# Kernel optimization log

Hardware: AMD Instinct MI355X
Metric: run time of the kernel (lower is better)

## Reference

```python
import jax, jax.numpy as jnp
import numpy as np

B, N, D, H, F = 16, 512, 768, 8, 96  # D == H*F, dims preserved across layers
NEG_INF = -1e20


def setup_inputs() -> dict:
    key = jax.random.key(0)
    ks = jax.random.split(key, 16)
    embeddings = jax.random.normal(ks[0], (B, N, D), dtype=jnp.float32)
    # 0/1 float adjacency with self-loops so no row is fully masked
    adj = (jax.random.uniform(ks[1], (B, N, N)) < 0.3).astype(jnp.float32)
    adj = jnp.maximum(adj, jnp.eye(N, dtype=jnp.float32)[None])
    convo_len = jnp.full((B,), N, dtype=jnp.int32)

    def layer_params(k0, k1, k2, k3, k4, in_dim, out_dim):
        sW = (2.0 / (in_dim + out_dim)) ** 0.5  # ~xavier
        sa = (2.0 / (out_dim + 1)) ** 0.5
        sH = (2.0 / (in_dim + in_dim)) ** 0.5
        return dict(
            W=jax.random.normal(k0, (H, in_dim, out_dim)) * sW,
            b=jnp.zeros((out_dim,), jnp.float32),
            a_src=jax.random.normal(k1, (H, out_dim, 1)) * sa,
            a_dst=jax.random.normal(k2, (H, out_dim, 1)) * sa,
            Hw=jax.random.normal(k3, (in_dim, in_dim)) * sH,
            Hb=jnp.zeros((in_dim,), jnp.float32),
        )

    p0 = layer_params(ks[2], ks[3], ks[4], ks[5], ks[6], D, F)
    p1 = layer_params(ks[7], ks[8], ks[9], ks[10], ks[11], D, F)
    return {
        "embeddings": embeddings, "adj": adj, "convo_len": convo_len,
        "W0": p0["W"], "b0": p0["b"], "a_src0": p0["a_src"], "a_dst0": p0["a_dst"], "Hw0": p0["Hw"], "Hb0": p0["Hb"],
        "W1": p1["W"], "b1": p1["b"], "a_src1": p1["a_src"], "a_dst1": p1["a_dst"], "Hw1": p1["Hw"], "Hb1": p1["Hb"],
    }


def gat_layer(x, adj, W, b, a_src, a_dst, Hw, Hb):
    b_, n_, _ = x.shape
    h_, _, f_ = W.shape
    h = jnp.einsum('bni,hio->bhno', x, W)            # [B,H,N,F]
    t = jnp.tanh(h)
    s = jnp.einsum('bhno,ho->bhn', t, a_src[..., 0])  # attn_src
    d = jnp.einsum('bhno,ho->bhn', t, a_dst[..., 0])  # attn_dst
    attn = jax.nn.leaky_relu(s[:, :, :, None] + d[:, :, None, :], 0.2)  # [B,H,N,N]
    attn = jnp.where(adj[:, None, :, :] > 0, attn, NEG_INF)
    attn = jax.nn.softmax(attn, axis=-1)
    out = jnp.einsum('bhij,bhjo->bhio', attn, h) + b  # [B,H,N,F]
    # faithful to torch: transpose(0,1).contiguous().view(batch, N, -1)
    out = jnp.transpose(out, (1, 0, 2, 3)).reshape(b_, n_, h_ * f_)
    out = jax.nn.elu(out)
    gate = jax.nn.sigmoid(x @ Hw.T + Hb)
    return gate * out + (1.0 - gate) * x


def reference(embeddings, adj, convo_len,
              W0, b0, a_src0, a_dst0, Hw0, Hb0,
              W1, b1, a_src1, a_dst1, Hw1, Hb1):
    x = gat_layer(embeddings, adj, W0, b0, a_src0, a_dst0, Hw0, Hb0)
    x = gat_layer(x, adj, W1, b1, a_src1, a_dst1, Hw1, Hb1)
    return x
```

## Files before the change

### kernel.cpp

```cpp
#include <hip/hip_runtime.h>
#include <cstdint>
#include <cstddef>

typedef __attribute__((ext_vector_type(4))) float f32x4;
typedef __attribute__((ext_vector_type(8))) __bf16 bf16x8;
typedef __attribute__((ext_vector_type(8))) unsigned short u16x8;
typedef __attribute__((ext_vector_type(4))) unsigned short u16x4;

__device__ __forceinline__ unsigned short f2bf(float f){
  unsigned int u = __float_as_uint(f);
  u += 0x7fffu + ((u >> 16) & 1u);
  return (unsigned short)(u >> 16);
}
__device__ __forceinline__ float bf2f(unsigned short u){
  return __uint_as_float(((unsigned int)u) << 16);
}
__device__ __forceinline__ float fast_tanh(float x){
  const float e = __expf(2.f * x);
  return 1.f - 2.f / (e + 1.f);
}

__device__ __forceinline__ void gload_lds16(const void* g, void* l){
  __builtin_amdgcn_global_load_lds((const __attribute__((address_space(1))) void*)g,
                                   (__attribute__((address_space(3))) void*)l, 16, 0, 0);
}

__device__ __forceinline__ f32x4 mfma16(bf16x8 a, bf16x8 b, f32x4 c){
  return __builtin_amdgcn_mfma_f32_16x16x32_bf16(a, b, c, 0, 0, 0);
}

#define SBAR()  { __builtin_amdgcn_sched_barrier(0); __builtin_amdgcn_s_barrier(); __builtin_amdgcn_sched_barrier(0); }

__global__ __launch_bounds__(256) void prep_kernel(const float* __restrict__ in,
                                                   unsigned short* __restrict__ out,
                                                   const float* __restrict__ adj,
                                                   unsigned int* __restrict__ mask,
                                                   const float* __restrict__ W0,
                                                   const float* __restrict__ Hw0,
                                                   unsigned short* __restrict__ Bt0,
                                                   const float* __restrict__ W1,
                                                   const float* __restrict__ Hw1,
                                                   unsigned short* __restrict__ Bt1){
  const int bid = blockIdx.x;
  if (bid < 6144){
    int i = bid * 256 + threadIdx.x;
    f32x4 v = ((const f32x4*)in)[i];
    union { unsigned short u[4]; unsigned long long ll; } o;
    #pragma unroll
    for (int e = 0; e < 4; ++e) o.u[e] = f2bf(v[e]);
    ((unsigned long long*)out)[i] = o.ll;
  } else if (bid < 6656){
    int idx = (bid - 6144) * 256 + threadIdx.x;
    const float* a = adj + (size_t)idx * 32;
    unsigned int m = 0;
    #pragma unroll
    for (int e = 0; e < 8; ++e){
      f32x4 v = *(const f32x4*)(a + e * 4);
      m |= (v[0] > 0.f ? 1u : 0u) << (e * 4);
      m |= (v[1] > 0.f ? 1u : 0u) << (e * 4 + 1);
      m |= (v[2] > 0.f ? 1u : 0u) << (e * 4 + 2);
      m |= (v[3] > 0.f ? 1u : 0u) << (e * 4 + 3);
    }
    mask[idx] = m;
  } else {
    const int rel = bid - 6656;
    const int layer = rel >= 1536;
    const int n = layer ? rel - 1536 : rel;
    const float* W  = layer ? W1  : W0;
    const float* Hw = layer ? Hw1 : Hw0;
    unsigned short* Bt = layer ? Bt1 : Bt0;
    const int k4 = threadIdx.x;
    if (k4 < 192){
      float v[4];
      if (n < 768){
        int head = n / 96, f = n % 96;
        const float* base = W + (size_t)head * 768 * 96 + f;
        #pragma unroll
        for (int e = 0; e < 4; ++e) v[e] = base[(size_t)(k4 * 4 + e) * 96];
      } else {
        f32x4 t = *(const f32x4*)(Hw + (size_t)(n - 768) * 768 + k4 * 4);
        #pragma unroll
        for (int e = 0; e < 4; ++e) v[e] = t[e];
      }
      union { unsigned short u[4]; unsigned long long ll; } o;
      #pragma unroll
      for (int e = 0; e < 4; ++e) o.u[e] = f2bf(v[e]);
      ((unsigned long long*)(Bt + (size_t)n * 768))[k4] = o.ll;
    }
  }
}

__global__ __launch_bounds__(256, 3)
void gemm_kernel(const unsigned short* __restrict__ A,
                 const unsigned short* __restrict__ Bt,
                 const float* __restrict__ Hb,
                 unsigned short* __restrict__ hT,
                 unsigned short* __restrict__ glogit){
  __shared__ __align__(16) char lds[49152];
  const int tid  = threadIdx.x;
  const int wid  = tid >> 6;
  const int lane = tid & 63;
  const int orig = blockIdx.x;
  const int wgid = (orig & 7) * 192 + (orig >> 3);
  const int mtile = wgid / 24, ntile = wgid % 24;
  const int m0 = mtile * 128, n0 = ntile * 64;
  const int wm = (wid >> 1) * 64, wn = (wid & 1) * 32;
  const int g = lane >> 4, r16 = lane & 15;

  auto stage = [&](int kt, char* base){
    #pragma unroll
    for (int c = 0; c < 4; ++c){
      const int ch = c * 256 + tid;
      const int row = ch >> 3, sp = ch & 7;
      const int cj = sp ^ (row & 7);
      gload_lds16(A + (size_t)(m0 + row) * 768 + kt * 64 + cj * 8, base + ch * 16);
    }
    #pragma unroll
    for (int c = 0; c < 2; ++c){
      const int ch = c * 256 + tid;
      const int row = ch >> 3, sp = ch & 7;
      const int cj = sp ^ (row & 7);
      gload_lds16(Bt + (size_t)(n0 + row) * 768 + kt * 64 + cj * 8, base + 16384 + ch * 16);
    }
  };

  f32x4 acc[4][2];
  #pragma unroll
  for (int i = 0; i < 4; ++i)
    #pragma unroll
    for (int j = 0; j < 2; ++j) acc[i][j] = (f32x4){0.f, 0.f, 0.f, 0.f};

  stage(0, lds);
  stage(1, lds + 24576);

  for (int kt = 0; kt < 12; ++kt){
    if (kt < 11) { asm volatile("s_waitcnt vmcnt(6)" ::: "memory"); }
    else         { asm volatile("s_waitcnt vmcnt(0)" ::: "memory"); }
    SBAR();
    const char* base = lds + (kt & 1) * 24576;
    bf16x8 af[4][2], bfr[2][2];
    #pragma unroll
    for (int t = 0; t < 4; ++t){
      const int rowA = wm + t * 16 + r16;
      #pragma unroll
      for (int kk = 0; kk < 2; ++kk){
        const int ckk = (kk << 2) | g;
        af[t][kk] = *(const bf16x8*)(base + rowA * 128 + ((ckk ^ (rowA & 7)) << 4));
      }
    }
    #pragma unroll
    for (int nt = 0; nt < 2; ++nt){
      const int rowB = wn + nt * 16 + r16;
      #pragma unroll
      for (int kk = 0; kk < 2; ++kk){
        const int ckk = (kk << 2) | g;
        bfr[nt][kk] = *(const bf16x8*)(base + 16384 + rowB * 128 + ((ckk ^ (rowB & 7)) << 4));
      }
    }
    __builtin_amdgcn_s_setprio(1);
    #pragma unroll
    for (int mt = 0; mt < 4; ++mt)
      #pragma unroll
      for (int nt = 0; nt < 2; ++nt){
        acc[mt][nt] = mfma16(af[mt][0], bfr[nt][0], acc[mt][nt]);
        acc[mt][nt] = mfma16(af[mt][1], bfr[nt][1], acc[mt][nt]);
      }
    __builtin_amdgcn_s_setprio(0);
    SBAR();
    if (kt < 10) stage(kt + 2, lds + (kt & 1) * 24576);
  }

  if (n0 < 768){
    #pragma unroll
    for (int mt = 0; mt < 4; ++mt){
      #pragma unroll
      for (int nt = 0; nt < 2; ++nt){
        const int n_local = wn + nt * 16 + r16;
        const int m_base  = wm + mt * 16 + g * 4;
        union { unsigned short u[4]; unsigned long long ll; } pk;
        #pragma unroll
        for (int r = 0; r < 4; ++r) pk.u[r] = f2bf(acc[mt][nt][r]);
        const int byte = m_base * 2;
        const int chunk = byte >> 4, o = byte & 15;
        const int pbyte = n_local * 256 + ((chunk ^ (n_local & 15)) << 4) + o;
        *(unsigned long long*)(lds + pbyte) = pk.ll;
      }
    }
    __syncthreads();
    const int b_ = m0 >> 9, nodebase = m0 & 511;
    #pragma unroll
    for (int it = 0; it < 4; ++it){
      const int ci = it * 256 + tid;
      const int row = ci >> 4, l = ci & 15;
      const int pbyte = row * 256 + (((l ^ (row & 15))) << 4);
      f32x4 v = *(const f32x4*)(lds + pbyte);
      const int n = n0 + row, head = n / 96, f = n % 96;
      *(f32x4*)(hT + (((size_t)(b_ * 8 + head)) * 96 + f) * 512 + nodebase + l * 8) = v;
    }
  } else {
    #pragma unroll
    for (int mt = 0; mt < 4; ++mt){
      #pragma unroll
      for (int nt = 0; nt < 2; ++nt){
        const int n_local = wn + nt * 16 + r16;
        const float hbv = Hb[n0 - 768 + n_local];
        const int c = n_local >> 3;
        #pragma unroll
        for (int r = 0; r < 4; ++r){
          const int m_local = wm + mt * 16 + g * 4 + r;
          const int pbyte = m_local * 128 + ((c ^ (m_local & 7)) << 4) + (n_local & 7) * 2;
          *(unsigned short*)(lds + pbyte) = f2bf(acc[mt][nt][r] + hbv);
        }
      }
    }
    __syncthreads();
    const int colbase = n0 - 768;
    #pragma unroll
    for (int it = 0; it < 4; ++it){
      const int ci = it * 256 + tid;
      const int row = ci >> 3, l = ci & 7;
      const int pbyte = row * 128 + ((l ^ (row & 7)) << 4);
      f32x4 v = *(const f32x4*)(lds + pbyte);
      *(f32x4*)(glogit + (size_t)(m0 + row) * 768 + colbase + l * 8) = v;
    }
  }
}

__global__ __launch_bounds__(256)
void sd_kernel(const unsigned short* __restrict__ hT, const float* __restrict__ asrc,
               const float* __restrict__ adst, float* __restrict__ s, float* __restrict__ d){
  const int bh = blockIdx.x;
  const int tid = threadIdx.x;
  const int head = bh & 7;
  __shared__ float as_lds[96], ad_lds[96];
  if (tid < 96) as_lds[tid] = asrc[head * 96 + tid];
  else if (tid >= 128 && tid < 224) ad_lds[tid - 128] = adst[head * 96 + tid - 128];
  __syncthreads();

  const unsigned short* hTb = hT + (size_t)bh * 96 * 512 + tid * 2;
  float s0 = 0.f, s1 = 0.f, d0 = 0.f, d1 = 0.f;
  #pragma unroll 8
  for (int f = 0; f < 96; ++f){
    const unsigned int u = *(const unsigned int*)(hTb + (size_t)f * 512);
    const float t0 = fast_tanh(bf2f((unsigned short)(u & 0xffffu)));
    const float t1 = fast_tanh(bf2f((unsigned short)(u >> 16)));
    const float a = as_lds[f], dd = ad_lds[f];
    s0 += t0 * a;  s1 += t1 * a;
    d0 += t0 * dd; d1 += t1 * dd;
  }
  const int o = (bh << 9) + tid * 2;
  *(float2*)(s + o) = make_float2(s0, s1);
  *(float2*)(d + o) = make_float2(d0, d1);
}

__global__ __launch_bounds__(256)
void attn_kernel(const float* __restrict__ s, const float* __restrict__ d,
                 const unsigned int* __restrict__ mask,
                 const unsigned short* __restrict__ hT,
                 const float* __restrict__ bias,
                 const unsigned short* __restrict__ glogit,
                 const float* __restrict__ xin,
                 float* __restrict__ outf,
                 unsigned short* __restrict__ outb,
                 int write_b){
  const int idx = blockIdx.x;
  const int bh = idx & 127, ib = idx >> 7;
  const int b  = bh >> 3;
  const int tid = threadIdx.x, wid = tid >> 6, lane = tid & 63;
  const int g = lane >> 4, r16 = lane & 15;
  const int rowbase = ib * 64 + wid * 16;

  __shared__ float d_lds[512];
  __shared__ float bias_lds[96];
  __shared__ __align__(16) char vbuf[3][12288];
  float* att_s = (float*)vbuf;

  const float* dv = d + bh * 512;
  if (tid < 128) ((f32x4*)d_lds)[tid] = ((const f32x4*)dv)[tid];
  if (tid >= 128 && tid < 152) ((f32x4*)bias_lds)[tid - 128] = ((const f32x4*)bias)[tid - 128];

  const unsigned short* hTb = hT + (size_t)bh * 96 * 512;

  auto stage = [&](int p, int bufi){
    #pragma unroll
    for (int ss2 = 0; ss2 < 3; ++ss2){
      const int ch = ss2 * 256 + tid;
      const int row = ch >> 3, slotpos = ch & 7;
      const int cj = slotpos ^ (row & 7);
      gload_lds16(hTb + (size_t)row * 512 + p * 64 + cj * 8, vbuf[bufi] + ch * 16);
    }
  };

  const int i_mine = rowbase + r16;
  const float s_i = s[bh * 512 + i_mine];

  unsigned int mw[16];
  {
    const uint4* mrow = (const uint4*)(mask + ((size_t)b * 512 + i_mine) * 16);
    uint4 a0 = mrow[0], a1 = mrow[1], a2 = mrow[2], a3 = mrow[3];
    mw[0]=a0.x; mw[1]=a0.y; mw[2]=a0.z; mw[3]=a0.w;
    mw[4]=a1.x; mw[5]=a1.y; mw[6]=a1.z; mw[7]=a1.w;
    mw[8]=a2.x; mw[9]=a2.y; mw[10]=a2.z; mw[11]=a2.w;
    mw[12]=a3.x; mw[13]=a3.y; mw[14]=a3.z; mw[15]=a3.w;
  }

  stage(0, 0);
  stage(1, 1);
  asm volatile("s_waitcnt lgkmcnt(0)" ::: "memory");

  float m_i;
  f32x4 acc2[6];
  #pragma unroll
  for (int ft = 0; ft < 6; ++ft) acc2[ft] = (f32x4){0.f, 0.f, 0.f, 0.f};
  float L0 = 0.f, L1 = 0.f, L2 = 0.f, L3 = 0.f;

  #pragma unroll
  for (int p = 0; p < 8; ++p){
    if (p < 7) { asm volatile("s_waitcnt vmcnt(3)" ::: "memory"); }
    else       { asm volatile("s_waitcnt vmcnt(0)" ::: "memory"); }
    SBAR();
    if (p == 0){
      float Mx = d_lds[lane];
      #pragma unroll
      for (int t = 1; t < 8; ++t) Mx = fmaxf(Mx, d_lds[t * 64 + lane]);
      #pragma unroll
      for (int o = 32; o > 0; o >>= 1) Mx = fmaxf(Mx, __shfl_xor(Mx, o));
      const float scm = s_i + Mx;
      m_i = fmaxf(scm, 0.2f * scm);
    }
    if (p < 6) stage(p + 2, (p + 2) % 3);
    const char* vb = vbuf[p % 3];
    #pragma unroll
    for (int half = 0; half < 2; ++half){
      const int jt = p * 2 + half;
      const unsigned int w = mw[jt];
      const int j8 = jt * 32 + g * 8;
      f32x4 dA = *(const f32x4*)(d_lds + j8);
      f32x4 dB = *(const f32x4*)(d_lds + j8 + 4);
      u16x8 pa;
      #pragma unroll
      for (int e = 0; e < 4; ++e){
        float sc = s_i + dA[e]; sc = fmaxf(sc, 0.2f * sc);
        float p1 = ((w >> (g * 8 + e)) & 1u) ? __expf(sc - m_i) : 0.f;
        float sc2 = s_i + dB[e]; sc2 = fmaxf(sc2, 0.2f * sc2);
        float p2 = ((w >> (g * 8 + 4 + e)) & 1u) ? __expf(sc2 - m_i) : 0.f;
        if (e == 0){ L0 += p1; L0 += p2; } else if (e == 1){ L1 += p1; L1 += p2; }
        else if (e == 2){ L2 += p1; L2 += p2; } else { L3 += p1; L3 += p2; }
        pa[e] = f2bf(p1);
        pa[4 + e] = f2bf(p2);
      }
      const bf16x8 af = __builtin_bit_cast(bf16x8, pa);
      const int slot = ((half * 4 + g) ^ (r16 & 7)) * 16;
      __builtin_amdgcn_s_setprio(1);
      #pragma unroll
      for (int ft = 0; ft < 6; ++ft){
        bf16x8 vf = *(const bf16x8*)(vb + (ft * 16 + r16) * 128 + slot);
        acc2[ft] = mfma16(af, vf, acc2[ft]);
      }
      __builtin_amdgcn_s_setprio(0);
    }
  }
  __syncthreads();

  float L = (L0 + L1) + (L2 + L3);
  L += __shfl_xor(L, 16);
  L += __shfl_xor(L, 32);
  const float linv = 1.f / L;
  float lr[4];
  #pragma unroll
  for (int r = 0; r < 4; ++r) lr[r] = __shfl(linv, g * 4 + r);

  #pragma unroll
  for (int ft = 0; ft < 6; ++ft){
    const int f = ft * 16 + r16;
    const float bv = bias_lds[f];
    #pragma unroll
    for (int r = 0; r < 4; ++r){
      const int node = rowbase + g * 4 + r;
      att_s[((node >> 3) & 7) * 768 + (node & 7) * 96 + f] = acc2[ft][r] * lr[r] + bv;
    }
  }
  __syncthreads();

  const int hh = bh & 7;
  const int bb2 = (hh << 1) | (b >> 3);
  const int mbase = bb2 * 512 + ((b & 7) << 6) + ib * 8;
  const size_t gb4 = (size_t)mbase * 192;
  #pragma unroll
  for (int sgi = 0; sgi < 6; ++sgi){
    const int ei = sgi * 256 + tid;
    f32x4 a4 = ((const f32x4*)att_s)[ei];
    u16x4 gl = ((const u16x4*)glogit)[gb4 + ei];
    f32x4 xv = ((const f32x4*)xin)[gb4 + ei];
    f32x4 o;
    #pragma unroll
    for (int e = 0; e < 4; ++e){
      const float gate = 1.f / (1.f + __expf(-bf2f(gl[e])));
      const float a = a4[e];
      const float eluv = a > 0.f ? a : (__expf(a) - 1.f);
      o[e] = gate * eluv + (1.f - gate) * xv[e];
    }
    ((f32x4*)outf)[gb4 + ei] = o;
    if (write_b){
      union { unsigned short u[4]; unsigned long long ll; } ob;
      #pragma unroll
      for (int e = 0; e < 4; ++e) ob.u[e] = f2bf(o[e]);
      ((unsigned long long*)outb)[gb4 + ei] = ob.ll;
    }
  }
}

extern "C" void kernel_launch(void* const* d_in, const int* in_sizes, int n_in,
                              void* d_out, int out_size, void* d_ws, size_t ws_size,
                              hipStream_t stream){
  const float* emb   = (const float*)d_in[0];
  const float* adj   = (const float*)d_in[1];
  const float* W0    = (const float*)d_in[3];
  const float* b0    = (const float*)d_in[4];
  const float* asrc0 = (const float*)d_in[5];
  const float* adst0 = (const float*)d_in[6];
  const float* Hw0   = (const float*)d_in[7];
  const float* Hb0   = (const float*)d_in[8];
  const float* W1    = (const float*)d_in[9];
  const float* b1    = (const float*)d_in[10];
  const float* asrc1 = (const float*)d_in[11];
  const float* adst1 = (const float*)d_in[12];
  const float* Hw1   = (const float*)d_in[13];
  const float* Hb1   = (const float*)d_in[14];

  char* ws = (char*)d_ws;
  size_t off = 0;
  auto alloc = [&](size_t bytes){ void* p = ws + off; off += (bytes + 255) & ~(size_t)255; return p; };
  unsigned short* x0b  = (unsigned short*)alloc(8192ull * 768 * 2);
  unsigned short* Bt0  = (unsigned short*)alloc(1536ull * 768 * 2);
  unsigned short* Bt1  = (unsigned short*)alloc(1536ull * 768 * 2);
  unsigned short* hT   = (unsigned short*)alloc(8192ull * 768 * 2);
  unsigned short* glogit = (unsigned short*)alloc(8192ull * 768 * 2);
  float* sbuf          = (float*)alloc(65536ull * 4);
  float* dbuf          = (float*)alloc(65536ull * 4);
  float* x1            = (float*)alloc(8192ull * 768 * 4);
  unsigned int* mask   = (unsigned int*)alloc(16ull * 512 * 16 * 4);
  (void)ws_size; (void)in_sizes; (void)n_in; (void)out_size;

  prep_kernel<<<9728, 256, 0, stream>>>(emb, x0b, adj, mask, W0, Hw0, Bt0, W1, Hw1, Bt1);

  gemm_kernel<<<1536, 256, 0, stream>>>(x0b, Bt0, Hb0, hT, glogit);
  sd_kernel<<<128, 256, 0, stream>>>(hT, asrc0, adst0, sbuf, dbuf);
  attn_kernel<<<1024, 256, 0, stream>>>(sbuf, dbuf, mask, hT, b0, glogit, emb, x1, x0b, 1);

  gemm_kernel<<<1536, 256, 0, stream>>>(x0b, Bt1, Hb1, hT, glogit);
  sd_kernel<<<128, 256, 0, stream>>>(hT, asrc1, adst1, sbuf, dbuf);
  attn_kernel<<<1024, 256, 0, stream>>>(sbuf, dbuf, mask, hT, b1, glogit, x1, (float*)d_out, x0b, 0);
}
```

Before: 246.7 us.

## Split attention key range across waves and load V directly from global

Restructures attn_kernel so each wave handles 32 rows over half of the key range, replacing the triple-buffered LDS staging of V with direct global loads into registers. Each V fragment is reused across two row groups. Partial accumulators and row sums from the two key halves are combined through an LDS reduction. The change cuts LDS footprint and adds launch_bounds occupancy hints, trading async LDS pipelining for direct vector loads plus an extra reduction step.

```diff
diff --git a/kernel.cpp b/kernel.cpp
--- a/kernel.cpp
+++ b/kernel.cpp
@@ -253,7 +253,7 @@
   *(float2*)(d + o) = make_float2(d0, d1);
 }
 
-__global__ __launch_bounds__(256)
+__global__ __launch_bounds__(256, 4)
 void attn_kernel(const float* __restrict__ s, const float* __restrict__ d,
                  const unsigned int* __restrict__ mask,
                  const unsigned short* __restrict__ hT,
@@ -267,13 +267,15 @@
   const int bh = idx & 127, ib = idx >> 7;
   const int b  = bh >> 3;
   const int tid = threadIdx.x, wid = tid >> 6, lane = tid & 63;
+  const int wi = wid >> 1, wj = wid & 1;
   const int g = lane >> 4, r16 = lane & 15;
-  const int rowbase = ib * 64 + wid * 16;
-
+
+  __shared__ __align__(16) char smem[25600];
   __shared__ float d_lds[512];
   __shared__ float bias_lds[96];
-  __shared__ __align__(16) char vbuf[3][12288];
-  float* att_s = (float*)vbuf;
+  __shared__ float Lred[2][2][16];
+  float* red   = (float*)smem;
+  float* att_s = (float*)smem;
 
   const float* dv = d + bh * 512;
   if (tid < 128) ((f32x4*)d_lds)[tid] = ((const f32x4*)dv)[tid];
@@ -281,103 +283,126 @@
 
   const unsigned short* hTb = hT + (size_t)bh * 96 * 512;
 
-  auto stage = [&](int p, int bufi){
-    #pragma unroll
-    for (int ss2 = 0; ss2 < 3; ++ss2){
-      const int ch = ss2 * 256 + tid;
-      const int row = ch >> 3, slotpos = ch & 7;
-      const int cj = slotpos ^ (row & 7);
-      gload_lds16(hTb + (size_t)row * 512 + p * 64 + cj * 8, vbuf[bufi] + ch * 16);
-    }
-  };
-
-  const int i_mine = rowbase + r16;
-  const float s_i = s[bh * 512 + i_mine];
-
-  unsigned int mw[16];
-  {
-    const uint4* mrow = (const uint4*)(mask + ((size_t)b * 512 + i_mine) * 16);
-    uint4 a0 = mrow[0], a1 = mrow[1], a2 = mrow[2], a3 = mrow[3];
-    mw[0]=a0.x; mw[1]=a0.y; mw[2]=a0.z; mw[3]=a0.w;
-    mw[4]=a1.x; mw[5]=a1.y; mw[6]=a1.z; mw[7]=a1.w;
-    mw[8]=a2.x; mw[9]=a2.y; mw[10]=a2.z; mw[11]=a2.w;
-    mw[12]=a3.x; mw[13]=a3.y; mw[14]=a3.z; mw[15]=a3.w;
-  }
-
-  stage(0, 0);
-  stage(1, 1);
-  asm volatile("s_waitcnt lgkmcnt(0)" ::: "memory");
-
-  float m_i;
-  f32x4 acc2[6];
-  #pragma unroll
-  for (int ft = 0; ft < 6; ++ft) acc2[ft] = (f32x4){0.f, 0.f, 0.f, 0.f};
-  float L0 = 0.f, L1 = 0.f, L2 = 0.f, L3 = 0.f;
-
-  #pragma unroll
-  for (int p = 0; p < 8; ++p){
-    if (p < 7) { asm volatile("s_waitcnt vmcnt(3)" ::: "memory"); }
-    else       { asm volatile("s_waitcnt vmcnt(0)" ::: "memory"); }
-    SBAR();
-    if (p == 0){
-      float Mx = d_lds[lane];
-      #pragma unroll
-      for (int t = 1; t < 8; ++t) Mx = fmaxf(Mx, d_lds[t * 64 + lane]);
-      #pragma unroll
-      for (int o = 32; o > 0; o >>= 1) Mx = fmaxf(Mx, __shfl_xor(Mx, o));
-      const float scm = s_i + Mx;
-      m_i = fmaxf(scm, 0.2f * scm);
-    }
-    if (p < 6) stage(p + 2, (p + 2) % 3);
-    const char* vb = vbuf[p % 3];
-    #pragma unroll
-    for (int half = 0; half < 2; ++half){
-      const int jt = p * 2 + half;
-      const unsigned int w = mw[jt];
-      const int j8 = jt * 32 + g * 8;
-      f32x4 dA = *(const f32x4*)(d_lds + j8);
-      f32x4 dB = *(const f32x4*)(d_lds + j8 + 4);
+  const int row0 = ib * 64 + wi * 32;
+  float s_i[2];
+  s_i[0] = s[bh * 512 + row0 + r16];
+  s_i[1] = s[bh * 512 + row0 + 16 + r16];
+
+  unsigned int mw[2][8];
+  #pragma unroll
+  for (int rg = 0; rg < 2; ++rg){
+    const uint4* mrow = (const uint4*)(mask + ((size_t)b * 512 + row0 + rg * 16 + r16) * 16 + wj * 8);
+    uint4 a0 = mrow[0], a1 = mrow[1];
+    mw[rg][0]=a0.x; mw[rg][1]=a0.y; mw[rg][2]=a0.z; mw[rg][3]=a0.w;
+    mw[rg][4]=a1.x; mw[rg][5]=a1.y; mw[rg][6]=a1.z; mw[rg][7]=a1.w;
+  }
+
+  __syncthreads();
+
+  float Mx = d_lds[lane];
+  #pragma unroll
+  for (int t = 1; t < 8; ++t) Mx = fmaxf(Mx, d_lds[t * 64 + lane]);
+  #pragma unroll
+  for (int o = 32; o > 0; o >>= 1) Mx = fmaxf(Mx, __shfl_xor(Mx, o));
+  float m_i[2];
+  #pragma unroll
+  for (int rg = 0; rg < 2; ++rg){
+    const float scm = s_i[rg] + Mx;
+    m_i[rg] = fmaxf(scm, 0.2f * scm);
+  }
+
+  f32x4 acc[2][6];
+  #pragma unroll
+  for (int rg = 0; rg < 2; ++rg)
+    #pragma unroll
+    for (int ft = 0; ft < 6; ++ft) acc[rg][ft] = (f32x4){0.f, 0.f, 0.f, 0.f};
+  float L[2] = {0.f, 0.f};
+
+  #pragma unroll
+  for (int jt = 0; jt < 8; ++jt){
+    const int j8 = wj * 256 + jt * 32 + g * 8;
+    bf16x8 vf[6];
+    #pragma unroll
+    for (int ft = 0; ft < 6; ++ft)
+      vf[ft] = *(const bf16x8*)(hTb + (size_t)(ft * 16 + r16) * 512 + j8);
+
+    f32x4 dA = *(const f32x4*)(d_lds + j8);
+    f32x4 dB = *(const f32x4*)(d_lds + j8 + 4);
+    #pragma unroll
+    for (int rg = 0; rg < 2; ++rg){
+      const unsigned int w = mw[rg][jt];
       u16x8 pa;
       #pragma unroll
       for (int e = 0; e < 4; ++e){
-        float sc = s_i + dA[e]; sc = fmaxf(sc, 0.2f * sc);
-        float p1 = ((w >> (g * 8 + e)) & 1u) ? __expf(sc - m_i) : 0.f;
-        float sc2 = s_i + dB[e]; sc2 = fmaxf(sc2, 0.2f * sc2);
-        float p2 = ((w >> (g * 8 + 4 + e)) & 1u) ? __expf(sc2 - m_i) : 0.f;
-        if (e == 0){ L0 += p1; L0 += p2; } else if (e == 1){ L1 += p1; L1 += p2; }
-        else if (e == 2){ L2 += p1; L2 += p2; } else { L3 += p1; L3 += p2; }
+        float sc = s_i[rg] + dA[e]; sc = fmaxf(sc, 0.2f * sc);
+        float p1 = ((w >> (g * 8 + e)) & 1u) ? __expf(sc - m_i[rg]) : 0.f;
+        float sc2 = s_i[rg] + dB[e]; sc2 = fmaxf(sc2, 0.2f * sc2);
+        float p2 = ((w >> (g * 8 + 4 + e)) & 1u) ? __expf(sc2 - m_i[rg]) : 0.f;
+        L[rg] += p1; L[rg] += p2;
         pa[e] = f2bf(p1);
         pa[4 + e] = f2bf(p2);
       }
       const bf16x8 af = __builtin_bit_cast(bf16x8, pa);
-      const int slot = ((half * 4 + g) ^ (r16 & 7)) * 16;
       __builtin_amdgcn_s_setprio(1);
       #pragma unroll
+      for (int ft = 0; ft < 6; ++ft)
+        acc[rg][ft] = mfma16(af, vf[ft], acc[rg][ft]);
+      __builtin_amdgcn_s_setprio(0);
+    }
+  }
+
+  #pragma unroll
+  for (int rg = 0; rg < 2; ++rg){
+    L[rg] += __shfl_xor(L[rg], 16);
+    L[rg] += __shfl_xor(L[rg], 32);
+  }
+
+  if (wj == 1){
+    #pragma unroll
+    for (int rg = 0; rg < 2; ++rg){
+      #pragma unroll
+      for (int ft = 0; ft < 6; ++ft)
+        #pragma unroll
+        for (int r = 0; r < 4; ++r)
+          red[(size_t)wi * 3200 + (rg * 16 + g * 4 + r) * 100 + ft * 16 + r16] = acc[rg][ft][r];
+    }
+    if (lane < 16){ Lred[wi][0][lane] = L[0]; Lred[wi][1][lane] = L[1]; }
+  }
+  __syncthreads();
+  if (wj == 0){
+    #pragma unroll
+    for (int rg = 0; rg < 2; ++rg){
+      #pragma unroll
+      for (int ft = 0; ft < 6; ++ft)
+        #pragma unroll
+        for (int r = 0; r < 4; ++r)
+          acc[rg][ft][r] += red[(size_t)wi * 3200 + (rg * 16 + g * 4 + r) * 100 + ft * 16 + r16];
+    }
+    L[0] += Lred[wi][0][r16];
+    L[1] += Lred[wi][1][r16];
+  }
+  __syncthreads();
+
+  if (wj == 0){
+    float lr[2][4];
+    #pragma unroll
+    for (int rg = 0; rg < 2; ++rg){
+      const float linv = 1.f / L[rg];
+      #pragma unroll
+      for (int r = 0; r < 4; ++r) lr[rg][r] = __shfl(linv, g * 4 + r);
+    }
+    #pragma unroll
+    for (int rg = 0; rg < 2; ++rg){
+      #pragma unroll
       for (int ft = 0; ft < 6; ++ft){
-        bf16x8 vf = *(const bf16x8*)(vb + (ft * 16 + r16) * 128 + slot);
-        acc2[ft] = mfma16(af, vf, acc2[ft]);
-      }
-      __builtin_amdgcn_s_setprio(0);
-    }
-  }
-  __syncthreads();
-
-  float L = (L0 + L1) + (L2 + L3);
-  L += __shfl_xor(L, 16);
-  L += __shfl_xor(L, 32);
-  const float linv = 1.f / L;
-  float lr[4];
-  #pragma unroll
-  for (int r = 0; r < 4; ++r) lr[r] = __shfl(linv, g * 4 + r);
-
-  #pragma unroll
-  for (int ft = 0; ft < 6; ++ft){
-    const int f = ft * 16 + r16;
-    const float bv = bias_lds[f];
-    #pragma unroll
-    for (int r = 0; r < 4; ++r){
-      const int node = rowbase + g * 4 + r;
-      att_s[((node >> 3) & 7) * 768 + (node & 7) * 96 + f] = acc2[ft][r] * lr[r] + bv;
+        const int f = ft * 16 + r16;
+        const float bv = bias_lds[f];
+        #pragma unroll
+        for (int r = 0; r < 4; ++r){
+          const int node = row0 + rg * 16 + g * 4 + r;
+          att_s[((node >> 3) & 7) * 768 + (node & 7) * 96 + f] = acc[rg][ft][r] * lr[rg][r] + bv;
+        }
+      }
     }
   }
   __syncthreads();
```

Result: slower. 415.5 us (+68.4%).

## Fuse attention score projections into GEMM epilogue and use bf16 residual input

Applied to the files above, without the earlier changes.

The separate sd_kernel is removed. The tanh(h)·a_src and tanh(h)·a_dst reductions are now computed in the GEMM epilogue from the fp32 accumulators: each wave reduces its part with shuffles and adds it into zero-initialised s/d buffers with atomicAdd. prep_kernel gains extra blocks that clear those buffers. The attention kernel also reads the residual x from the bf16 copy instead of fp32, and layer 0 no longer writes an fp32 intermediate, which cuts global memory traffic and one launch per layer. In exchange it adds atomic contention, order-dependent float sums, and lower precision in the gate residual path.

```diff
diff --git a/kernel.cpp b/kernel.cpp
--- a/kernel.cpp
+++ b/kernel.cpp
@@ -40,7 +40,8 @@
                                                    unsigned short* __restrict__ Bt0,
                                                    const float* __restrict__ W1,
                                                    const float* __restrict__ Hw1,
-                                                   unsigned short* __restrict__ Bt1){
+                                                   unsigned short* __restrict__ Bt1,
+                                                   float* __restrict__ sdzero){
   const int bid = blockIdx.x;
   if (bid < 6144){
     int i = bid * 256 + threadIdx.x;
@@ -62,7 +63,7 @@
       m |= (v[3] > 0.f ? 1u : 0u) << (e * 4 + 3);
     }
     mask[idx] = m;
-  } else {
+  } else if (bid < 9728){
     const int rel = bid - 6656;
     const int layer = rel >= 1536;
     const int n = layer ? rel - 1536 : rel;
@@ -87,6 +88,9 @@
       for (int e = 0; e < 4; ++e) o.u[e] = f2bf(v[e]);
       ((unsigned long long*)(Bt + (size_t)n * 768))[k4] = o.ll;
     }
+  } else {
+    const int i = (bid - 9728) * 256 + threadIdx.x;
+    ((f32x4*)sdzero)[i] = (f32x4){0.f, 0.f, 0.f, 0.f};
   }
 }
 
@@ -94,8 +98,12 @@
 void gemm_kernel(const unsigned short* __restrict__ A,
                  const unsigned short* __restrict__ Bt,
                  const float* __restrict__ Hb,
+                 const float* __restrict__ asrc,
+                 const float* __restrict__ adst,
                  unsigned short* __restrict__ hT,
-                 unsigned short* __restrict__ glogit){
+                 unsigned short* __restrict__ glogit,
+                 float* __restrict__ sdst,
+                 float* __restrict__ ddst){
   __shared__ __align__(16) char lds[49152];
   const int tid  = threadIdx.x;
   const int wid  = tid >> 6;
@@ -171,6 +179,34 @@
   }
 
   if (n0 < 768){
+    const int headu = (n0 + wn) / 96;
+    const int bb_ = m0 >> 9;
+    #pragma unroll
+    for (int mt = 0; mt < 4; ++mt){
+      float accs[4] = {0.f,0.f,0.f,0.f}, accd[4] = {0.f,0.f,0.f,0.f};
+      #pragma unroll
+      for (int nt = 0; nt < 2; ++nt){
+        const int n = n0 + wn + nt * 16 + r16;
+        const float av = asrc[n], adv = adst[n];
+        #pragma unroll
+        for (int r = 0; r < 4; ++r){
+          const float t = fast_tanh(acc[mt][nt][r]);
+          accs[r] += t * av; accd[r] += t * adv;
+        }
+      }
+      #pragma unroll
+      for (int r = 0; r < 4; ++r){
+        float ssv = accs[r], ddv = accd[r];
+        #pragma unroll
+        for (int o = 8; o > 0; o >>= 1){ ssv += __shfl_xor(ssv, o); ddv += __shfl_xor(ddv, o); }
+        if (r16 == 0){
+          const int m = m0 + wm + mt * 16 + g * 4 + r;
+          const int oix = ((bb_ * 8 + headu) << 9) + (m & 511);
+          atomicAdd(sdst + oix, ssv);
+          atomicAdd(ddst + oix, ddv);
+        }
+      }
+    }
     #pragma unroll
     for (int mt = 0; mt < 4; ++mt){
       #pragma unroll
@@ -227,42 +263,15 @@
 }
 
 __global__ __launch_bounds__(256)
-void sd_kernel(const unsigned short* __restrict__ hT, const float* __restrict__ asrc,
-               const float* __restrict__ adst, float* __restrict__ s, float* __restrict__ d){
-  const int bh = blockIdx.x;
-  const int tid = threadIdx.x;
-  const int head = bh & 7;
-  __shared__ float as_lds[96], ad_lds[96];
-  if (tid < 96) as_lds[tid] = asrc[head * 96 + tid];
-  else if (tid >= 128 && tid < 224) ad_lds[tid - 128] = adst[head * 96 + tid - 128];
-  __syncthreads();
-
-  const unsigned short* hTb = hT + (size_t)bh * 96 * 512 + tid * 2;
-  float s0 = 0.f, s1 = 0.f, d0 = 0.f, d1 = 0.f;
-  #pragma unroll 8
-  for (int f = 0; f < 96; ++f){
-    const unsigned int u = *(const unsigned int*)(hTb + (size_t)f * 512);
-    const float t0 = fast_tanh(bf2f((unsigned short)(u & 0xffffu)));
-    const float t1 = fast_tanh(bf2f((unsigned short)(u >> 16)));
-    const float a = as_lds[f], dd = ad_lds[f];
-    s0 += t0 * a;  s1 += t1 * a;
-    d0 += t0 * dd; d1 += t1 * dd;
-  }
-  const int o = (bh << 9) + tid * 2;
-  *(float2*)(s + o) = make_float2(s0, s1);
-  *(float2*)(d + o) = make_float2(d0, d1);
-}
-
-__global__ __launch_bounds__(256)
 void attn_kernel(const float* __restrict__ s, const float* __restrict__ d,
                  const unsigned int* __restrict__ mask,
                  const unsigned short* __restrict__ hT,
                  const float* __restrict__ bias,
                  const unsigned short* __restrict__ glogit,
-                 const float* __restrict__ xin,
+                 const unsigned short* __restrict__ xin,
                  float* __restrict__ outf,
                  unsigned short* __restrict__ outb,
-                 int write_b){
+                 int write_f, int write_b){
   const int idx = blockIdx.x;
   const int bh = idx & 127, ib = idx >> 7;
   const int b  = bh >> 3;
@@ -391,16 +400,16 @@
     const int ei = sgi * 256 + tid;
     f32x4 a4 = ((const f32x4*)att_s)[ei];
     u16x4 gl = ((const u16x4*)glogit)[gb4 + ei];
-    f32x4 xv = ((const f32x4*)xin)[gb4 + ei];
+    u16x4 xv = ((const u16x4*)xin)[gb4 + ei];
     f32x4 o;
     #pragma unroll
     for (int e = 0; e < 4; ++e){
       const float gate = 1.f / (1.f + __expf(-bf2f(gl[e])));
       const float a = a4[e];
       const float eluv = a > 0.f ? a : (__expf(a) - 1.f);
-      o[e] = gate * eluv + (1.f - gate) * xv[e];
-    }
-    ((f32x4*)outf)[gb4 + ei] = o;
+      o[e] = gate * eluv + (1.f - gate) * bf2f(xv[e]);
+    }
+    if (write_f) ((f32x4*)outf)[gb4 + ei] = o;
     if (write_b){
       union { unsigned short u[4]; unsigned long long ll; } ob;
       #pragma unroll
@@ -436,19 +445,18 @@
   unsigned short* Bt1  = (unsigned short*)alloc(1536ull * 768 * 2);
   unsigned short* hT   = (unsigned short*)alloc(8192ull * 768 * 2);
   unsigned short* glogit = (unsigned short*)alloc(8192ull * 768 * 2);
-  float* sbuf          = (float*)alloc(65536ull * 4);
-  float* dbuf          = (float*)alloc(65536ull * 4);
-  float* x1            = (float*)alloc(8192ull * 768 * 4);
+  float* sd0           = (float*)alloc(2ull * 65536 * 4);
+  float* sd1           = (float*)alloc(2ull * 65536 * 4);
   unsigned int* mask   = (unsigned int*)alloc(16ull * 512 * 16 * 4);
+  float* s0 = sd0, *d0 = sd0 + 65536;
+  float* s1 = sd1, *d1 = sd1 + 65536;
   (void)ws_size; (void)in_sizes; (void)n_in; (void)out_size;
 
-  prep_kernel<<<9728, 256, 0, stream>>>(emb, x0b, adj, mask, W0, Hw0, Bt0, W1, Hw1, Bt1);
-
-  gemm_kernel<<<1536, 256, 0, stream>>>(x0b, Bt0, Hb0, hT, glogit);
-  sd_kernel<<<128, 256, 0, stream>>>(hT, asrc0, adst0, sbuf, dbuf);
-  attn_kernel<<<1024, 256, 0, stream>>>(sbuf, dbuf, mask, hT, b0, glogit, emb, x1, x0b, 1);
-
-  gemm_kernel<<<1536, 256, 0, stream>>>(x0b, Bt1, Hb1, hT, glogit);
-  sd_kernel<<<128, 256, 0, stream>>>(hT, asrc1, adst1, sbuf, dbuf);
-  attn_kernel<<<1024, 256, 0, stream>>>(sbuf, dbuf, mask, hT, b1, glogit, x1, (float*)d_out, x0b, 0);
-}
+  prep_kernel<<<9984, 256, 0, stream>>>(emb, x0b, adj, mask, W0, Hw0, Bt0, W1, Hw1, Bt1, sd0);
+
+  gemm_kernel<<<1536, 256, 0, stream>>>(x0b, Bt0, Hb0, asrc0, adst0, hT, glogit, s0, d0);
+  attn_kernel<<<1024, 256, 0, stream>>>(s0, d0, mask, hT, b0, glogit, x0b, (float*)d_out, x0b, 0, 1);
+
+  gemm_kernel<<<1536, 256, 0, stream>>>(x0b, Bt1, Hb1, asrc1, adst1, hT, glogit, s1, d1);
+  attn_kernel<<<1024, 256, 0, stream>>>(s1, d1, mask, hT, b1, glogit, x0b, (float*)d_out, x0b, 1, 0);
+}
```

New measurement: 239.9 us. 2.8% less time.
